# Kernel tuning notes

Hardware: AMD Instinct MI355X
Metric: run time of the kernel (lower is better)

Reference implementation:

```python
import jax, jax.numpy as jnp
import numpy as np

EMB = 64
D = 2 * EMB          # 128, feature dim of R / hidden of attention MLP
B, L = 128, 4096     # batch, sequence length
N_ITER = 50          # bisection iterations (entmax_bisect default)


def entmax_bisect(X, alpha, n_iter=N_ITER):
    """alpha-entmax via bisection over the last axis. X: [B, L], alpha: [B, 1] (>1)."""
    am1 = alpha - 1.0
    Xs = X * am1
    d = X.shape[-1]
    inv = 1.0 / am1
    max_val = jnp.max(Xs, axis=-1, keepdims=True)
    tau_lo0 = max_val - 1.0                       # gp(1, alpha) = 1
    tau_hi = max_val - (1.0 / d) ** am1           # gp(1/d, alpha)

    def p(tau):
        return jnp.clip(Xs - tau, 0.0, None) ** inv

    f_lo = jnp.sum(p(tau_lo0), axis=-1, keepdims=True) - 1.0

    def body(i, carry):
        tau_lo, dm, _ = carry
        dm = dm * 0.5
        tau_m = tau_lo + dm
        f_m = jnp.sum(p(tau_m), axis=-1, keepdims=True) - 1.0
        tau_lo = jnp.where(f_m * f_lo >= 0, tau_m, tau_lo)
        return (tau_lo, dm, tau_m)

    _, _, tau_m = jax.lax.fori_loop(0, n_iter, body, (tau_lo0, tau_hi - tau_lo0, tau_lo0))
    p_m = p(tau_m)
    return p_m / jnp.sum(p_m, axis=-1, keepdims=True)  # ensure_sum_one


def setup_inputs() -> dict:
    key = jax.random.key(0)
    ks = jax.random.split(key, 9)
    s = 1.0 / np.sqrt(D)
    R = jax.random.normal(ks[0], (B, L, D), dtype=jnp.float32)
    alpha = 1.25 + 0.5 * jax.random.uniform(ks[1], (B, 1), dtype=jnp.float32)  # in (1.25, 1.75)
    target = jax.random.normal(ks[2], (B, 1, D), dtype=jnp.float32)
    Wr1 = s * jax.random.normal(ks[3], (D, D), dtype=jnp.float32)      # Linear(2E, 2E), no bias
    Wr2 = s * jax.random.normal(ks[4], (D, EMB), dtype=jnp.float32)    # Linear(E, 2E) (shape-fixed), no bias
    Wr3 = s * jax.random.normal(ks[5], (1, D), dtype=jnp.float32)      # Linear(2E, 1), no bias
    bias_r = s * jax.random.normal(ks[6], (D,), dtype=jnp.float32)
    Wf_w = s * jax.random.normal(ks[7], (EMB, D), dtype=jnp.float32)   # Linear(2E, E)
    Wf_b = s * jax.random.normal(ks[8], (EMB,), dtype=jnp.float32)
    return {"R": R, "alpha": alpha, "target": target, "Wr1": Wr1, "Wr2": Wr2,
            "Wr3": Wr3, "bias_r": bias_r, "Wf_w": Wf_w, "Wf_b": Wf_b}


def reference(R, alpha, target, Wr1, Wr2, Wr3, bias_r, Wf_w, Wf_b):
    # q = Wf(target): [B, 1, E]
    q = jnp.einsum('btd,ed->bte', target, Wf_w) + Wf_b
    # additive attention score: Wr3 @ relu(Wr1 k + Wr2 q + b): [B, L]
    h = jax.nn.relu(jnp.einsum('bld,ed->ble', R, Wr1)
                    + jnp.einsum('bte,de->btd', q, Wr2)
                    + bias_r)
    scores = jnp.einsum('bld,d->bl', h, Wr3[0])
    # entmax sparsification over the sequence axis
    a = entmax_bisect(scores, alpha)
    # weighted sum of v = R: [B, D]
    res = jnp.einsum('bl,bld->bd', a, R)
    res = jax.nn.selu(res)
    res = res / jnp.linalg.norm(res, axis=-1, keepdims=True)
    return res
```

## Files before the change

### kernel.cpp

```cpp
#include <hip/hip_runtime.h>
#include <hip/hip_bf16.h>

#define B_ 128
#define L_ 4096
#define D_ 128
#define E_ 64

typedef __attribute__((ext_vector_type(8))) short short8;
typedef __attribute__((ext_vector_type(4))) float floatx4;

static __device__ __forceinline__ void split_trunc(float x, unsigned short& hs,
                                                   unsigned short& ls) {
  unsigned int bx = __float_as_uint(x);
  float hf = __uint_as_float(bx & 0xffff0000u);
  hs = (unsigned short)(bx >> 16);
  float lo = x - hf;
  ls = (unsigned short)(__float_as_uint(lo) >> 16);
}

__global__ __launch_bounds__(256, 2) void pass_b(
    const float* __restrict__ R, const float* __restrict__ alpha,
    const float* __restrict__ target, const float* __restrict__ Wr1,
    const float* __restrict__ Wr2, const float* __restrict__ Wr3,
    const float* __restrict__ bias_r, const float* __restrict__ Wf_w,
    const float* __restrict__ Wf_b, float* __restrict__ scores) {
  __shared__ __align__(16) unsigned short sAhi[16384];
  __shared__ __align__(16) unsigned short sAlo[16384];
  __shared__ float tg[D_];
  __shared__ float qv[E_];
  __shared__ float scvec[D_];

  const int b = blockIdx.x >> 5;
  const int lt = blockIdx.x & 31;
  const int t = threadIdx.x;
  const int wave = t >> 6, lane = t & 63;
  const int col = lane & 15, quad = lane >> 4;

  if (t < D_) tg[t] = target[b * D_ + t];

  const float* Rbase = R + ((size_t)b * L_ + (size_t)lt * 128) * D_;
  #pragma unroll
  for (int i = 0; i < 8; ++i) {
    const int mt = wave * 2 + (i >> 2);
    const int ks = i & 3;
    const int row = mt * 16 + col;
    const int c0 = ks * 32 + quad * 8;
    const float4* p = (const float4*)(Rbase + (size_t)row * D_ + c0);
    float4 v0 = p[0], v1 = p[1];
    float vv[8] = {v0.x, v0.y, v0.z, v0.w, v1.x, v1.y, v1.z, v1.w};
    union { unsigned short u[8]; short8 v; } H, Lo;
    #pragma unroll
    for (int j = 0; j < 8; ++j) split_trunc(vv[j], H.u[j], Lo.u[j]);
    const int base = ((mt * 4 + ks) * 64 + lane) * 8;
    *(short8*)(sAhi + base) = H.v;
    *(short8*)(sAlo + base) = Lo.v;
  }

  short8 bh[2][4], bl[2][4];
  #pragma unroll
  for (int n = 0; n < 2; ++n)
    #pragma unroll
    for (int ks = 0; ks < 4; ++ks) {
      const int e = (wave * 2 + n) * 16 + col;
      const int c0 = ks * 32 + quad * 8;
      const float4* p = (const float4*)(Wr1 + e * D_ + c0);
      float4 v0 = p[0], v1 = p[1];
      float vv[8] = {v0.x, v0.y, v0.z, v0.w, v1.x, v1.y, v1.z, v1.w};
      union { unsigned short u[8]; short8 v; } H, Lo;
      #pragma unroll
      for (int j = 0; j < 8; ++j) split_trunc(vv[j], H.u[j], Lo.u[j]);
      bh[n][ks] = H.v;
      bl[n][ks] = Lo.v;
    }

  floatx4 acc[8][2];
  #pragma unroll
  for (int mt = 0; mt < 8; ++mt)
    #pragma unroll
    for (int n = 0; n < 2; ++n) acc[mt][n] = (floatx4){0.f, 0.f, 0.f, 0.f};

  __syncthreads();

  if (t < E_) {
    float s = Wf_b[t];
    #pragma unroll 8
    for (int d = 0; d < D_; ++d) s += tg[d] * Wf_w[t * D_ + d];
    qv[t] = s;
  }
  __syncthreads();
  if (t < D_) {
    float s = bias_r[t];
    #pragma unroll 8
    for (int e = 0; e < E_; ++e) s += qv[e] * Wr2[t * E_ + e];
    scvec[t] = s;
  }

  #pragma unroll
  for (int mt = 0; mt < 8; ++mt) {
    #pragma unroll
    for (int ks = 0; ks < 4; ++ks) {
      const int ai = ((mt * 4 + ks) * 64 + lane) * 8;
      short8 ah = *(const short8*)(sAhi + ai);
      short8 al = *(const short8*)(sAlo + ai);
      #pragma unroll
      for (int n = 0; n < 2; ++n) {
        acc[mt][n] = __builtin_amdgcn_mfma_f32_16x16x32_bf16(ah, bh[n][ks], acc[mt][n], 0, 0, 0);
        acc[mt][n] = __builtin_amdgcn_mfma_f32_16x16x32_bf16(al, bh[n][ks], acc[mt][n], 0, 0, 0);
        acc[mt][n] = __builtin_amdgcn_mfma_f32_16x16x32_bf16(ah, bl[n][ks], acc[mt][n], 0, 0, 0);
      }
    }
  }

  __syncthreads();

  float w3[2], cb[2];
  #pragma unroll
  for (int n = 0; n < 2; ++n) {
    const int e = (wave * 2 + n) * 16 + col;
    w3[n] = Wr3[e];
    cb[n] = scvec[e];
  }
  float part[8][4];
  #pragma unroll
  for (int mt = 0; mt < 8; ++mt)
    #pragma unroll
    for (int r = 0; r < 4; ++r) {
      float s = 0.f;
      #pragma unroll
      for (int n = 0; n < 2; ++n)
        s += w3[n] * fmaxf(acc[mt][n][r] + cb[n], 0.f);
      s += __shfl_xor(s, 1, 64);
      s += __shfl_xor(s, 2, 64);
      s += __shfl_xor(s, 4, 64);
      s += __shfl_xor(s, 8, 64);
      part[mt][r] = s;
    }
  float* red = (float*)sAhi;
  if (col == 0) {
    #pragma unroll
    for (int mt = 0; mt < 8; ++mt)
      #pragma unroll
      for (int r = 0; r < 4; ++r)
        red[wave * 128 + mt * 16 + quad * 4 + r] = part[mt][r];
  }
  __syncthreads();
  if (t < 128) {
    float s = (red[t] + red[128 + t]) + (red[256 + t] + red[384 + t]);
    scores[(size_t)b * L_ + lt * 128 + t] = s;
  }
}

__global__ __launch_bounds__(512) void pass_cd(
    const float* __restrict__ scores, const float* __restrict__ alpha,
    const float* __restrict__ R, float* __restrict__ out) {
  const int b = blockIdx.x, t = threadIdx.x;
  const int wave = t >> 6, lane = t & 63;
  __shared__ float sred[2][8];
  __shared__ unsigned short sidx[L_];
  __shared__ float sw[L_];
  __shared__ float ppart[512];
  __shared__ int scnt;
  const float am1 = alpha[b] - 1.0f;
  const float inv = 1.0f / am1;
  const float* S = scores + (size_t)b * L_;
  float Xs[8];
  #pragma unroll
  for (int i = 0; i < 8; ++i) Xs[i] = S[i * 512 + t] * am1;
  if (t == 0) scnt = 0;

  float mx = Xs[0];
  #pragma unroll
  for (int i = 1; i < 8; ++i) mx = fmaxf(mx, Xs[i]);
  #pragma unroll
  for (int m = 32; m >= 1; m >>= 1) mx = fmaxf(mx, __shfl_xor(mx, m, 64));
  if (lane == 0) sred[0][wave] = mx;
  __syncthreads();
  mx = sred[0][0];
  #pragma unroll
  for (int w = 1; w < 8; ++w) mx = fmaxf(mx, sred[0][w]);

  float tau_lo = mx - 1.0f;
  float dm = (mx - exp2f(-12.0f * am1)) - tau_lo;

  int pc = 1;
  auto sumP = [&](float tau) -> float {
    const int par = pc & 1;
    ++pc;
    float s = 0.f;
    #pragma unroll
    for (int i = 0; i < 8; ++i) {
      float u = Xs[i] - tau;
      if (u > 0.f) s += exp2f(inv * __log2f(u));
    }
    #pragma unroll
    for (int m = 32; m >= 1; m >>= 1) s += __shfl_xor(s, m, 64);
    if (lane == 0) sred[par][wave] = s;
    __syncthreads();
    float r = sred[par][0];
    #pragma unroll
    for (int w = 1; w < 8; ++w) r += sred[par][w];
    return r;
  };

  const float f_lo = sumP(tau_lo) - 1.0f;
  float tau_m = tau_lo;
  for (int it = 0; it < 24; ++it) {
    dm *= 0.5f;
    tau_m = tau_lo + dm;
    float f_m = sumP(tau_m) - 1.0f;
    if (f_m * f_lo >= 0.f) tau_lo = tau_m;
  }

  float s = 0.f;
  #pragma unroll
  for (int i = 0; i < 8; ++i) {
    float u = Xs[i] - tau_m;
    if (u > 0.f) {
      float p = exp2f(inv * __log2f(u));
      s += p;
      int pos = atomicAdd(&scnt, 1);
      sidx[pos] = (unsigned short)(i * 512 + t);
      sw[pos] = p;
    }
  }
  {
    const int par = pc & 1;
    ++pc;
    #pragma unroll
    for (int m = 32; m >= 1; m >>= 1) s += __shfl_xor(s, m, 64);
    if (lane == 0) sred[par][wave] = s;
    __syncthreads();
    s = sred[par][0];
    #pragma unroll
    for (int w = 1; w < 8; ++w) s += sred[par][w];
  }
  const int ns = scnt;
  const float rs = 1.0f / s;

  const float* Rb = R + (size_t)b * L_ * D_;
  const int g = t >> 7, c = t & 127;
  float acc = 0.f;
  int k = g;
  for (; k + 4 < ns; k += 8) {
    int i0 = sidx[k], i1 = sidx[k + 4];
    float w0 = sw[k], w1 = sw[k + 4];
    acc += w0 * Rb[(size_t)i0 * D_ + c] + w1 * Rb[(size_t)i1 * D_ + c];
  }
  for (; k < ns; k += 4) acc += sw[k] * Rb[(size_t)sidx[k] * D_ + c];
  __syncthreads();
  ppart[t] = acc;
  __syncthreads();
  float r = 0.f;
  if (t < 128) {
    float a2 = ((ppart[t] + ppart[t + 128]) + (ppart[t + 256] + ppart[t + 384])) * rs;
    const float sc = 1.0507009873554805f, al = 1.6732632423543772f;
    r = a2 > 0.f ? sc * a2 : sc * al * (expf(a2) - 1.0f);
  }
  float q = r * r;
  #pragma unroll
  for (int m = 32; m >= 1; m >>= 1) q += __shfl_xor(q, m, 64);
  if (lane == 0) sred[0][wave] = q;
  __syncthreads();
  if (t < 128) {
    float nrm = sqrtf(sred[0][0] + sred[0][1]);
    out[b * D_ + t] = r / nrm;
  }
}

extern "C" void kernel_launch(void* const* d_in, const int* in_sizes, int n_in,
                              void* d_out, int out_size, void* d_ws, size_t ws_size,
                              hipStream_t stream) {
  const float* R      = (const float*)d_in[0];
  const float* alpha  = (const float*)d_in[1];
  const float* target = (const float*)d_in[2];
  const float* Wr1    = (const float*)d_in[3];
  const float* Wr2    = (const float*)d_in[4];
  const float* Wr3    = (const float*)d_in[5];
  const float* bias_r = (const float*)d_in[6];
  const float* Wf_w   = (const float*)d_in[7];
  const float* Wf_b   = (const float*)d_in[8];
  float* out = (float*)d_out;

  float* scores = (float*)d_ws;

  hipLaunchKernelGGL(pass_b, dim3(B_ * 32), dim3(256), 0, stream,
                     R, alpha, target, Wr1, Wr2, Wr3, bias_r, Wf_w, Wf_b, scores);
  hipLaunchKernelGGL(pass_cd, dim3(B_), dim3(512), 0, stream,
                     scores, alpha, R, out);
}
```

Before: 493.2 us.

## Hoist weight split and query projection into prep kernel; shrink score tiles

Adds a prep kernel that splits Wr1 once into bf16 hi/lo fragments in MFMA layout and computes the per-batch bias vector (Wf projection plus Wr2 plus bias) once per batch. Before, each of the 32 score blocks per batch redid this work. pass_b now loads the pre-split fragments and the bias vector, and each block handles 64 rows instead of 128. The smaller tiles halve LDS use and raise the occupancy hint to 4, which should hide more of the R load latency. The cost is an extra kernel launch, more blocks, and each block reloading Wr1 fragments from global memory.

```diff
diff --git a/kernel.cpp b/kernel.cpp
--- a/kernel.cpp
+++ b/kernel.cpp
@@ -18,32 +18,66 @@
   ls = (unsigned short)(__float_as_uint(lo) >> 16);
 }
 
-__global__ __launch_bounds__(256, 2) void pass_b(
-    const float* __restrict__ R, const float* __restrict__ alpha,
-    const float* __restrict__ target, const float* __restrict__ Wr1,
-    const float* __restrict__ Wr2, const float* __restrict__ Wr3,
-    const float* __restrict__ bias_r, const float* __restrict__ Wf_w,
-    const float* __restrict__ Wf_b, float* __restrict__ scores) {
-  __shared__ __align__(16) unsigned short sAhi[16384];
-  __shared__ __align__(16) unsigned short sAlo[16384];
-  __shared__ float tg[D_];
-  __shared__ float qv[E_];
-  __shared__ float scvec[D_];
-
-  const int b = blockIdx.x >> 5;
-  const int lt = blockIdx.x & 31;
+__global__ __launch_bounds__(256) void prep(
+    const float* __restrict__ Wr1, unsigned short* __restrict__ hi,
+    unsigned short* __restrict__ lo, const float* __restrict__ target,
+    const float* __restrict__ Wr2, const float* __restrict__ bias_r,
+    const float* __restrict__ Wf_w, const float* __restrict__ Wf_b,
+    float* __restrict__ cvec) {
+  if (blockIdx.x < 64) {
+    int t = blockIdx.x * 256 + threadIdx.x;
+    int j = t & 7, lane = (t >> 3) & 63, ks = (t >> 9) & 3, nt = t >> 11;
+    int e = nt * 16 + (lane & 15);
+    int d = ks * 32 + (lane >> 4) * 8 + j;
+    split_trunc(Wr1[e * D_ + d], hi[t], lo[t]);
+  } else {
+    const int sub = threadIdx.x >> 7;
+    const int t = threadIdx.x & 127;
+    const int b = (blockIdx.x - 64) * 2 + sub;
+    __shared__ float tg[2][D_];
+    __shared__ float q[2][E_];
+    tg[sub][t] = target[b * D_ + t];
+    __syncthreads();
+    if (t < E_) {
+      float s = Wf_b[t];
+      #pragma unroll 8
+      for (int d = 0; d < D_; ++d) s += tg[sub][d] * Wf_w[t * D_ + d];
+      q[sub][t] = s;
+    }
+    __syncthreads();
+    float s = bias_r[t];
+    #pragma unroll 8
+    for (int e = 0; e < E_; ++e) s += q[sub][e] * Wr2[t * E_ + e];
+    cvec[b * D_ + t] = s;
+  }
+}
+
+__global__ __launch_bounds__(256, 4) void pass_b(
+    const float* __restrict__ R, const unsigned short* __restrict__ Whi,
+    const unsigned short* __restrict__ Wlo, const float* __restrict__ cvec,
+    const float* __restrict__ Wr3, float* __restrict__ scores) {
+  __shared__ __align__(16) unsigned short sAhi[8192];
+  __shared__ __align__(16) unsigned short sAlo[8192];
+  __shared__ float red[256];
+
+  const int b = blockIdx.x >> 6;
+  const int lt = blockIdx.x & 63;
   const int t = threadIdx.x;
   const int wave = t >> 6, lane = t & 63;
   const int col = lane & 15, quad = lane >> 4;
 
-  if (t < D_) tg[t] = target[b * D_ + t];
-
-  const float* Rbase = R + ((size_t)b * L_ + (size_t)lt * 128) * D_;
-  #pragma unroll
-  for (int i = 0; i < 8; ++i) {
-    const int mt = wave * 2 + (i >> 2);
-    const int ks = i & 3;
-    const int row = mt * 16 + col;
+  float w3[2], cb[2];
+  #pragma unroll
+  for (int n = 0; n < 2; ++n) {
+    const int e = (wave * 2 + n) * 16 + col;
+    w3[n] = Wr3[e];
+    cb[n] = cvec[b * D_ + e];
+  }
+
+  const float* Rbase = R + ((size_t)b * L_ + (size_t)lt * 64) * D_;
+  #pragma unroll
+  for (int ks = 0; ks < 4; ++ks) {
+    const int row = wave * 16 + col;
     const int c0 = ks * 32 + quad * 8;
     const float4* p = (const float4*)(Rbase + (size_t)row * D_ + c0);
     float4 v0 = p[0], v1 = p[1];
@@ -51,7 +85,7 @@
     union { unsigned short u[8]; short8 v; } H, Lo;
     #pragma unroll
     for (int j = 0; j < 8; ++j) split_trunc(vv[j], H.u[j], Lo.u[j]);
-    const int base = ((mt * 4 + ks) * 64 + lane) * 8;
+    const int base = ((wave * 4 + ks) * 64 + lane) * 8;
     *(short8*)(sAhi + base) = H.v;
     *(short8*)(sAlo + base) = Lo.v;
   }
@@ -61,42 +95,21 @@
   for (int n = 0; n < 2; ++n)
     #pragma unroll
     for (int ks = 0; ks < 4; ++ks) {
-      const int e = (wave * 2 + n) * 16 + col;
-      const int c0 = ks * 32 + quad * 8;
-      const float4* p = (const float4*)(Wr1 + e * D_ + c0);
-      float4 v0 = p[0], v1 = p[1];
-      float vv[8] = {v0.x, v0.y, v0.z, v0.w, v1.x, v1.y, v1.z, v1.w};
-      union { unsigned short u[8]; short8 v; } H, Lo;
-      #pragma unroll
-      for (int j = 0; j < 8; ++j) split_trunc(vv[j], H.u[j], Lo.u[j]);
-      bh[n][ks] = H.v;
-      bl[n][ks] = Lo.v;
-    }
-
-  floatx4 acc[8][2];
-  #pragma unroll
-  for (int mt = 0; mt < 8; ++mt)
+      const int off = (((wave * 2 + n) * 4 + ks) * 64 + lane) * 8;
+      bh[n][ks] = *(const short8*)(Whi + off);
+      bl[n][ks] = *(const short8*)(Wlo + off);
+    }
+
+  floatx4 acc[4][2];
+  #pragma unroll
+  for (int mt = 0; mt < 4; ++mt)
     #pragma unroll
     for (int n = 0; n < 2; ++n) acc[mt][n] = (floatx4){0.f, 0.f, 0.f, 0.f};
 
   __syncthreads();
 
-  if (t < E_) {
-    float s = Wf_b[t];
-    #pragma unroll 8
-    for (int d = 0; d < D_; ++d) s += tg[d] * Wf_w[t * D_ + d];
-    qv[t] = s;
-  }
-  __syncthreads();
-  if (t < D_) {
-    float s = bias_r[t];
-    #pragma unroll 8
-    for (int e = 0; e < E_; ++e) s += qv[e] * Wr2[t * E_ + e];
-    scvec[t] = s;
-  }
-
-  #pragma unroll
-  for (int mt = 0; mt < 8; ++mt) {
+  #pragma unroll
+  for (int mt = 0; mt < 4; ++mt) {
     #pragma unroll
     for (int ks = 0; ks < 4; ++ks) {
       const int ai = ((mt * 4 + ks) * 64 + lane) * 8;
@@ -111,18 +124,9 @@
     }
   }
 
-  __syncthreads();
-
-  float w3[2], cb[2];
-  #pragma unroll
-  for (int n = 0; n < 2; ++n) {
-    const int e = (wave * 2 + n) * 16 + col;
-    w3[n] = Wr3[e];
-    cb[n] = scvec[e];
-  }
-  float part[8][4];
-  #pragma unroll
-  for (int mt = 0; mt < 8; ++mt)
+  float part[4][4];
+  #pragma unroll
+  for (int mt = 0; mt < 4; ++mt)
     #pragma unroll
     for (int r = 0; r < 4; ++r) {
       float s = 0.f;
@@ -135,18 +139,18 @@
       s += __shfl_xor(s, 8, 64);
       part[mt][r] = s;
     }
-  float* red = (float*)sAhi;
+  __syncthreads();
   if (col == 0) {
     #pragma unroll
-    for (int mt = 0; mt < 8; ++mt)
+    for (int mt = 0; mt < 4; ++mt)
       #pragma unroll
       for (int r = 0; r < 4; ++r)
-        red[wave * 128 + mt * 16 + quad * 4 + r] = part[mt][r];
-  }
-  __syncthreads();
-  if (t < 128) {
-    float s = (red[t] + red[128 + t]) + (red[256 + t] + red[384 + t]);
-    scores[(size_t)b * L_ + lt * 128 + t] = s;
+        red[wave * 64 + mt * 16 + quad * 4 + r] = part[mt][r];
+  }
+  __syncthreads();
+  if (t < 64) {
+    float s = (red[t] + red[64 + t]) + (red[128 + t] + red[192 + t]);
+    scores[(size_t)b * L_ + lt * 64 + t] = s;
   }
 }
 
@@ -281,10 +285,16 @@
   const float* Wf_b   = (const float*)d_in[8];
   float* out = (float*)d_out;
 
-  float* scores = (float*)d_ws;
-
-  hipLaunchKernelGGL(pass_b, dim3(B_ * 32), dim3(256), 0, stream,
-                     R, alpha, target, Wr1, Wr2, Wr3, bias_r, Wf_w, Wf_b, scores);
+  char* ws = (char*)d_ws;
+  float* cvec          = (float*)ws;
+  unsigned short* whi  = (unsigned short*)(ws + 65536);
+  unsigned short* wlo  = (unsigned short*)(ws + 98304);
+  float* scores        = (float*)(ws + 131072);
+
+  hipLaunchKernelGGL(prep, dim3(128), dim3(256), 0, stream,
+                     Wr1, whi, wlo, target, Wr2, bias_r, Wf_w, Wf_b, cvec);
+  hipLaunchKernelGGL(pass_b, dim3(B_ * 64), dim3(256), 0, stream,
+                     R, whi, wlo, cvec, Wr3, scores);
   hipLaunchKernelGGL(pass_cd, dim3(B_), dim3(512), 0, stream,
                      scores, alpha, R, out);
 }
```

After: 427.9 us. 13.2% less time.
